# Optimization experiments

Measured on AMD Instinct MI355X. Metric: run time of the kernel, lower is better.

The kernel has to match this reference:

```python
import jax, jax.numpy as jnp
import numpy as np

VOCAB, EMB, HID = 5000, 16, 32
B, T = 256, 2048


def setup_inputs() -> dict:
    key = jax.random.key(0)
    k1, k2, k3, k4, k5 = jax.random.split(key, 5)
    tokens = jax.random.randint(k1, (B, T), 0, VOCAB, dtype=jnp.int32)
    emb = jax.random.normal(k2, (VOCAB, EMB), dtype=jnp.float32) * 0.05
    Wk = jax.random.normal(k3, (EMB, 4 * HID), dtype=jnp.float32) * 0.1
    Wr = jax.random.normal(k4, (HID, 4 * HID), dtype=jnp.float32) * 0.1
    b = jax.random.normal(k5, (4 * HID,), dtype=jnp.float32) * 0.1
    return {"tokens": tokens, "emb": emb, "Wk": Wk, "Wr": Wr, "b": b}


def reference(tokens, emb, Wk, Wr, b):
    # Embedding lookup: [B, T, EMB]
    x = emb[tokens]
    # Mask: Keras Masking on tiled token values -> masked where token == 0.
    mask = (tokens != 0)  # [B, T] True = valid step
    # Precompute input projections for all timesteps: [B, T, 4H]
    zx = jnp.einsum('bte,eh->bth', x, Wk) + b
    zx_t = jnp.swapaxes(zx, 0, 1)        # [T, B, 4H]
    mask_t = jnp.swapaxes(mask, 0, 1)    # [T, B]

    def step(carry, inp):
        h, c = carry
        z_x, m = inp
        z = z_x + h @ Wr                      # [B, 4H]
        i, f, g, o = jnp.split(z, 4, axis=-1) # Keras gate order i,f,g,o
        i = jax.nn.sigmoid(i)
        f = jax.nn.sigmoid(f)
        g = jnp.tanh(g)
        o = jax.nn.sigmoid(o)
        c_new = f * c + i * g
        h_new = o * jnp.tanh(c_new)
        m = m[:, None]
        # Keras masked RNN: masked steps carry forward previous state/output
        h = jnp.where(m, h_new, h)
        c = jnp.where(m, c_new, c)
        return (h, c), h

    h0 = jnp.zeros((tokens.shape[0], HID), dtype=zx.dtype)
    c0 = jnp.zeros((tokens.shape[0], HID), dtype=zx.dtype)
    _, hs = jax.lax.scan(step, (h0, c0), (zx_t, mask_t))
    return jnp.swapaxes(hs, 0, 1)  # [B, T, HID]
```

## Files before the change

### kernel.cpp

```cpp
#include <hip/hip_runtime.h>

#define G    128
#define HID  32
#define EMB  16
#define BB   256
#define TT   2048
#define VOC  5000

#define LOG2E      1.44269504088896340736f
#define TWOLOG2E   2.88539008177792681472f

typedef float v2f __attribute__((ext_vector_type(2)));
typedef __attribute__((ext_vector_type(8))) short short8;
typedef __attribute__((ext_vector_type(4))) float f32x4;

__device__ __forceinline__ float bf2f(unsigned short u) {
    return __uint_as_float(((unsigned)u) << 16);
}
__device__ __forceinline__ unsigned short f2bf(float f) {
    unsigned x = __float_as_uint(f);
    return (unsigned short)((x + 0x7FFFu + ((x >> 16) & 1u)) >> 16);
}
__device__ __forceinline__ float sigm2(float x) {
    const float e = __builtin_amdgcn_exp2f(-x);
    return __builtin_amdgcn_rcpf(1.f + e);
}
__device__ __forceinline__ float sigm(float x) {
    const float e = __expf(-x);
    return __builtin_amdgcn_rcpf(1.f + e);
}
__device__ __forceinline__ float tanh_f(float x) {
    const float e = __expf(-2.f * x);
    return (1.f - e) * __builtin_amdgcn_rcpf(1.f + e);
}
__device__ __forceinline__ float rdlf(float v, int k) {
    return __int_as_float(__builtin_amdgcn_readlane(__float_as_int(v), k));
}
template <int CTRL>
__device__ __forceinline__ unsigned dppq_u(unsigned v) {
    return (unsigned)__builtin_amdgcn_update_dpp(0, (int)v, CTRL, 0xF, 0xF, true);
}
template <int CTRL>
__device__ __forceinline__ float dppq_f(float v) {
    return __uint_as_float(dppq_u<CTRL>(__float_as_uint(v)));
}
#define DPP_XOR2   0x4E
#define DPP_BODD   0xF5
#define DPP_BEVN   0xA0
#define DPP_HMIRR  0x141
#define DPP_ROR8   0x128
#define DPP_MIRR   0x140

__device__ __host__ __forceinline__ int col_a(int l) {
    return (l >> 1) + 32 * (l & 1);
}

__global__ __launch_bounds__(64) void detect_kernel(
    const unsigned int* __restrict__ bias_w, int* __restrict__ flag)
{
    const int l = threadIdx.x;
    const unsigned u  = bias_w[l];
    const unsigned lo = u & 0xFFFFu;
    const float vlo = __uint_as_float(lo << 16);
    const float vhi = __uint_as_float(u & 0xFFFF0000u);
    const bool nz_even = (lo != 0u);
    const bool big = !(fabsf(vlo) < 1e6f) || !(fabsf(vhi) < 1e6f);
    const unsigned long long nz = __ballot(nz_even);
    const unsigned long long bg = __ballot(big);
    if (l == 0 && blockIdx.x == 0)
        *flag = (nz == 0ull || bg != 0ull) ? 1 : 0;
}

#define ZK_RPB 8
__global__ __launch_bounds__(64) void zk_kernel(
    const void* __restrict__ emb, const void* __restrict__ Wk,
    const void* __restrict__ bias, float* __restrict__ ZK,
    const int* __restrict__ flag)
{
    const int l  = threadIdx.x;
    const int v0 = blockIdx.x * ZK_RPB;
    const bool f32 = flag[0] != 0;
    const int ca = col_a(l), cb = ca + 64;
    const float sa = LOG2E;
    const float sb = ((l & 1) == 0) ? 2.f * LOG2E : LOG2E;

    float wa[EMB], wb[EMB], ba, bb;
    if (f32) {
        const float* W = (const float*)Wk;
        const float* B = (const float*)bias;
#pragma unroll
        for (int e = 0; e < EMB; ++e) { wa[e] = W[e * G + ca]; wb[e] = W[e * G + cb]; }
        ba = B[ca]; bb = B[cb];
    } else {
        const unsigned short* W = (const unsigned short*)Wk;
        const unsigned short* B = (const unsigned short*)bias;
#pragma unroll
        for (int e = 0; e < EMB; ++e) { wa[e] = bf2f(W[e * G + ca]); wb[e] = bf2f(W[e * G + cb]); }
        ba = bf2f(B[ca]); bb = bf2f(B[cb]);
    }

#pragma unroll
    for (int r = 0; r < ZK_RPB; ++r) {
        const int v = v0 + r;
        float x[EMB];
        if (f32) {
            const float* E = (const float*)emb + (size_t)v * EMB;
#pragma unroll
            for (int e = 0; e < EMB; ++e) x[e] = E[e];
        } else {
            const unsigned short* E = (const unsigned short*)emb + (size_t)v * EMB;
#pragma unroll
            for (int e = 0; e < EMB; ++e) x[e] = bf2f(E[e]);
        }
        float za = ba, zb = bb;
#pragma unroll
        for (int e = 0; e < EMB; ++e) {
            za = fmaf(x[e], wa[e], za);
            zb = fmaf(x[e], wb[e], zb);
        }
        ZK[(size_t)v * G + 2 * l]     = za * sa;
        ZK[(size_t)v * G + 2 * l + 1] = zb * sb;
    }
}

template <bool F32OUT>
__device__ __forceinline__ void scan_zk_loop(
    const int* __restrict__ trow, const float* __restrict__ ZK,
    void* __restrict__ orow, const short8 (&Bf)[8], int lane)
{
    const bool  h0  = (lane & 1) == 0;
    const float gm  = h0 ? 2.f : 1.f, ga = h0 ? -1.f : 0.f;
    const int   oj  = lane >> 1;
    const int   g4  = (lane >> 4) & 3;
    const bool  u_odd = (lane >> 1) & 1;
    const unsigned psel = u_odd ? 0x03020706u : 0x07060302u;
    const int   lm  = lane & 15;

    const f32x4 zc = {0.f, 0.f, 0.f, 0.f};
    float h = 0.f, c = 0.f;

    int tva = trow[lm];
    int tvb = trow[16 + lm];
    int tc[16], tn[16];
#pragma unroll
    for (int p = 0; p < 16; ++p) tc[p] = __builtin_amdgcn_readlane(tva, p);
#pragma unroll
    for (int p = 0; p < 16; ++p) tn[p] = __builtin_amdgcn_readlane(tvb, p);

    v2f pz[8];
#pragma unroll
    for (int d = 0; d < 8; ++d)
        pz[d] = *(const v2f*)(ZK + (size_t)tc[d] * G + 2 * lane);

    for (int cc = 0; cc < TT / 16; ++cc) {
        const int base = cc * 16;
        const int nxtc = (cc + 2 < TT / 16) ? (cc + 2) : (TT / 16 - 1);
        const int tvc = trow[nxtc * 16 + lm];
#pragma unroll
        for (int u = 0; u < 16; ++u) {
            const int t = base + u;
            const v2f z = pz[u & 7];
            {
                const int ptok = (u + 8 < 16) ? tc[u + 8] : tn[u - 8];
                pz[u & 7] = *(const v2f*)(ZK + (size_t)ptok * G + 2 * lane);
            }

            const unsigned rh  = __float_as_uint(h) + 0x8000u;
            const unsigned prt = dppq_u<DPP_XOR2>(rh);
            const unsigned pair = __builtin_amdgcn_perm(prt, rh, psel);
            const unsigned q1 = dppq_u<DPP_HMIRR>(pair);
            const unsigned q2 = dppq_u<DPP_ROR8 >(pair);
            const unsigned q3 = dppq_u<DPP_MIRR >(pair);
            union { unsigned u4[4]; short8 s8; } au;
            au.u4[0] = pair; au.u4[1] = q1; au.u4[2] = q2; au.u4[3] = q3;
            const short8 Af = au.s8;

            f32x4 d0 = __builtin_amdgcn_mfma_f32_16x16x32_bf16(Af, Bf[0], zc, 0, 0, 0);
            f32x4 d1 = __builtin_amdgcn_mfma_f32_16x16x32_bf16(Af, Bf[1], zc, 0, 0, 0);
            f32x4 d2 = __builtin_amdgcn_mfma_f32_16x16x32_bf16(Af, Bf[2], zc, 0, 0, 0);
            f32x4 d3 = __builtin_amdgcn_mfma_f32_16x16x32_bf16(Af, Bf[3], zc, 0, 0, 0);
            f32x4 d4 = __builtin_amdgcn_mfma_f32_16x16x32_bf16(Af, Bf[4], zc, 0, 0, 0);
            f32x4 d5 = __builtin_amdgcn_mfma_f32_16x16x32_bf16(Af, Bf[5], zc, 0, 0, 0);
            f32x4 d6 = __builtin_amdgcn_mfma_f32_16x16x32_bf16(Af, Bf[6], zc, 0, 0, 0);
            f32x4 d7 = __builtin_amdgcn_mfma_f32_16x16x32_bf16(Af, Bf[7], zc, 0, 0, 0);

            const float mva = (g4 < 2) ? (g4 == 0 ? d0.x : d1.x)
                                       : (g4 == 2 ? d2.x : d3.x);
            const float mvb = (g4 < 2) ? (g4 == 0 ? d4.x : d5.x)
                                       : (g4 == 2 ? d6.x : d7.x);
            const float za = z.x + mva;
            const float zb = z.y + mvb;

            const float aa1 = sigm2(za);
            const float s2  = sigm2(zb);
            const float aam = aa1 * gm;
            const float qc  = aa1 * ga;
            const float q   = fmaf(aam, s2, qc);
            const float fG  = dppq_f<DPP_BODD>(aa1);
            const float oG  = dppq_f<DPP_BODD>(s2);
            const float pr  = dppq_f<DPP_BEVN>(q);
            const float cN  = fmaf(fG, c, pr);

            const float ex = __builtin_amdgcn_exp2f(cN * TWOLOG2E);
            const float rr = __builtin_amdgcn_rcpf(ex + 1.f);
            const float oo = oG + oG;
            const float hN = fmaf(-oo, rr, oG);

            const bool m = tc[u] != 0;
            c = m ? cN : c;
            h = m ? hN : h;

            const int oi = t * HID + oj;
            if (F32OUT) __builtin_nontemporal_store(h, (float*)orow + oi);
            else        __builtin_nontemporal_store(f2bf(h), (unsigned short*)orow + oi);
        }
#pragma unroll
        for (int p = 0; p < 16; ++p) tc[p] = tn[p];
#pragma unroll
        for (int p = 0; p < 16; ++p) tn[p] = __builtin_amdgcn_readlane(tvc, p);
    }
}

__global__ __launch_bounds__(64) void scan_zk_kernel(
    const int* __restrict__ tokens, const float* __restrict__ ZK,
    const void* __restrict__ Wr, const void* __restrict__ bias,
    void* __restrict__ out, const int* __restrict__ flag)
{
    const int lane = threadIdx.x, b = blockIdx.x;
    const bool f32 = flag[0] != 0;

    short8 Bf[8];
    const int n  = lane & 15;
    const int k0 = (lane >> 4) * 8;
#pragma unroll
    for (int p = 0; p < 8; ++p) {
        const int ell = 16 * (p & 3) + n;
        const int col = (p < 4) ? col_a(ell) : (col_a(ell) + 64);
        const int jx  = (p & 3) << 1;
        const float sc = (p >= 4 && (n & 1) == 0) ? 2.f * LOG2E : LOG2E;
        short el[8];
        if (f32) {
            const float* W = (const float*)Wr;
#pragma unroll
            for (int j = 0; j < 8; ++j)
                el[j] = (short)f2bf(W[(k0 + (j ^ jx)) * G + col] * sc);
        } else {
            const unsigned short* W = (const unsigned short*)Wr;
#pragma unroll
            for (int j = 0; j < 8; ++j)
                el[j] = (short)f2bf(bf2f(W[(k0 + (j ^ jx)) * G + col]) * sc);
        }
        short8 s;
#pragma unroll
        for (int j = 0; j < 8; ++j) s[j] = el[j];
        Bf[p] = s;
    }

    const int* trow = tokens + (size_t)b * TT;
    if (f32) scan_zk_loop<true >(trow, ZK, (char*)out + (size_t)b * TT * HID * 4, Bf, lane);
    else     scan_zk_loop<false>(trow, ZK, (char*)out + (size_t)b * TT * HID * 2, Bf, lane);
}

template <bool F32>
__device__ __forceinline__ void row_load(const void* emb, int tok, uint4* r) {
    if (F32) { const uint4* p = (const uint4*)((const float*)emb + (size_t)tok*EMB);
               r[0]=p[0]; r[1]=p[1]; r[2]=p[2]; r[3]=p[3]; }
    else     { const uint4* p = (const uint4*)((const unsigned short*)emb + (size_t)tok*EMB);
               r[0]=p[0]; r[1]=p[1]; }
}
template <bool F32>
__device__ __forceinline__ void row_unpack(const uint4* r, float* x) {
    if (F32) {
        const unsigned w[16] = {r[0].x,r[0].y,r[0].z,r[0].w, r[1].x,r[1].y,r[1].z,r[1].w,
                                r[2].x,r[2].y,r[2].z,r[2].w, r[3].x,r[3].y,r[3].z,r[3].w};
#pragma unroll
        for (int e = 0; e < 16; ++e) x[e] = __uint_as_float(w[e]);
    } else {
        const unsigned w[8] = {r[0].x,r[0].y,r[0].z,r[0].w, r[1].x,r[1].y,r[1].z,r[1].w};
#pragma unroll
        for (int q = 0; q < 8; ++q) {
            x[2*q]   = __uint_as_float(w[q] << 16);
            x[2*q+1] = __uint_as_float(w[q] & 0xFFFF0000u);
        }
    }
}

template <bool F32>
__device__ __forceinline__ void scan_fused_loop(
    const int* __restrict__ trow, const void* __restrict__ emb, void* orow,
    const float (&wka)[EMB], const float (&wkb)[EMB],
    const float (&wra)[HID], const float (&wrb)[HID],
    float za0, float zb0, const int* tl, int lane)
{
    const bool  lo  = lane < HID;
    const float zsc = lo ? 2.f : 1.f, gm = lo ? 2.f : 1.f, ga = lo ? -1.f : 0.f;
    float h = 0.f, c = 0.f;
    uint4 praw[2][4];
    row_load<F32>(emb, trow[0], praw[0]);
    row_load<F32>(emb, trow[1], praw[1]);

    for (int tt = 0; tt < TT; tt += 2) {
#pragma unroll
        for (int u = 0; u < 2; ++u) {
            const int t = tt + u;
            float x[EMB];
            row_unpack<F32>(praw[u], x);
            int tn = t + 2; tn = tn > TT - 1 ? TT - 1 : tn;
            row_load<F32>(emb, tl[tn], praw[u]);
            float za = za0, zb = zb0;
#pragma unroll
            for (int e = 0; e < EMB; ++e) { za = fmaf(x[e], wka[e], za); zb = fmaf(x[e], wkb[e], zb); }
#pragma unroll
            for (int k = 0; k < HID; ++k) {
                const float hk = rdlf(h, k);
                za = fmaf(hk, wra[k], za);
                zb = fmaf(hk, wrb[k], zb);
            }
            const float a1 = sigm(za);
            const float s2 = sigm(zb * zsc);
            const float a2 = fmaf(s2, gm, ga);
            const float x1 = __shfl_xor(a1, 32);
            const float x2 = __shfl_xor(a2, 32);
            const float iV = lo ? a1 : x1, fV = lo ? x1 : a1;
            const float gV = lo ? a2 : x2, oV = lo ? x2 : a2;
            const float cN = fmaf(fV, c, iV * gV);
            const float hN = oV * tanh_f(cN);
            const bool  m  = tl[t] != 0;
            c = m ? cN : c;
            h = m ? hN : h;
            const int oi = t * HID + (lane & (HID - 1));
            if (F32) ((float*)orow)[oi] = h;
            else     ((unsigned short*)orow)[oi] = f2bf(h);
        }
    }
}

__global__ __launch_bounds__(64) void scan_fused_kernel(
    const int* __restrict__ tokens, const void* __restrict__ emb,
    const void* __restrict__ Wk, const void* __restrict__ Wr,
    const void* __restrict__ bias, void* __restrict__ out,
    const int* __restrict__ flag, int defmode)
{
    __shared__ int tl[TT];
    const int lane = threadIdx.x, b = blockIdx.x;
    const bool f32 = flag ? (flag[0] != 0) : (defmode != 0);
    const int* trow = tokens + (size_t)b * TT;
    for (int t = lane; t < TT; t += 64) tl[t] = trow[t];

    float wka[EMB], wkb[EMB], wra[HID], wrb[HID], za0, zb0;
    if (f32) {
        const float* WK = (const float*)Wk; const float* WR = (const float*)Wr;
        const float* B  = (const float*)bias;
#pragma unroll
        for (int e = 0; e < EMB; ++e) { wka[e] = WK[e*G + lane]; wkb[e] = WK[e*G + lane + 64]; }
#pragma unroll
        for (int k = 0; k < HID; ++k) { wra[k] = WR[k*G + lane]; wrb[k] = WR[k*G + lane + 64]; }
        za0 = B[lane]; zb0 = B[lane + 64];
    } else {
        const unsigned short* WK = (const unsigned short*)Wk;
        const unsigned short* WR = (const unsigned short*)Wr;
        const unsigned short* B  = (const unsigned short*)bias;
#pragma unroll
        for (int e = 0; e < EMB; ++e) { wka[e] = bf2f(WK[e*G + lane]); wkb[e] = bf2f(WK[e*G + lane + 64]); }
#pragma unroll
        for (int k = 0; k < HID; ++k) { wra[k] = bf2f(WR[k*G + lane]); wrb[k] = bf2f(WR[k*G + lane + 64]); }
        za0 = bf2f(B[lane]); zb0 = bf2f(B[lane + 64]);
    }
    __syncthreads();

    if (f32) scan_fused_loop<true >(trow, emb, (char*)out + (size_t)b*TT*HID*4,
                                    wka, wkb, wra, wrb, za0, zb0, tl, lane);
    else     scan_fused_loop<false>(trow, emb, (char*)out + (size_t)b*TT*HID*2,
                                    wka, wkb, wra, wrb, za0, zb0, tl, lane);
}

extern "C" void kernel_launch(void* const* d_in, const int* in_sizes, int n_in,
                              void* d_out, int out_size, void* d_ws, size_t ws_size,
                              hipStream_t stream) {
    const int*  tokens = (const int*)d_in[0];
    const void* emb    = d_in[1];
    const void* Wk     = d_in[2];
    const void* Wr     = d_in[3];
    const void* bias   = d_in[4];

    const size_t zk_off   = 256;
    const size_t zk_bytes = (size_t)VOC * G * sizeof(float);

    if (ws_size >= zk_off + zk_bytes) {
        int*   flag = (int*)d_ws;
        float* ZK   = (float*)((char*)d_ws + zk_off);
        detect_kernel<<<1, 64, 0, stream>>>((const unsigned int*)bias, flag);
        zk_kernel<<<VOC / ZK_RPB, 64, 0, stream>>>(emb, Wk, bias, ZK, flag);
        scan_zk_kernel<<<BB, 64, 0, stream>>>(tokens, ZK, Wr, bias, d_out, flag);
    } else if (ws_size >= 16) {
        int* flag = (int*)d_ws;
        detect_kernel<<<1, 64, 0, stream>>>((const unsigned int*)bias, flag);
        scan_fused_kernel<<<BB, 64, 0, stream>>>(tokens, emb, Wk, Wr, bias, d_out, flag, 1);
    } else {
        scan_fused_kernel<<<BB, 64, 0, stream>>>(tokens, emb, Wk, Wr, bias, d_out, nullptr, 1);
    }
}
```

Measured before the change: 441.4 us.

## Fold gate input into MFMA accumulator and simplify LSTM activation algebra

Passes the precomputed input projection as the MFMA accumulator instead of adding it afterward. The sigmoid/tanh algebra is reworked so the cell state is carried in a pre-scaled domain, folding the constants into ZK precompute and rcp offsets, which removes several multiplies and adds from the serial recurrence. The separate detect kernel is also removed: each kernel now checks the bias dtype inline with a wave ballot, dropping one launch and the flag round-trip. The rescaled cell state and bf16 MFMA rounding could shift numerics slightly.

Result: slower. 492.6 us (+11.6%).

```diff
diff --git a/kernel.cpp b/kernel.cpp
--- a/kernel.cpp
+++ b/kernel.cpp
@@ -21,10 +21,6 @@
     unsigned x = __float_as_uint(f);
     return (unsigned short)((x + 0x7FFFu + ((x >> 16) & 1u)) >> 16);
 }
-__device__ __forceinline__ float sigm2(float x) {
-    const float e = __builtin_amdgcn_exp2f(-x);
-    return __builtin_amdgcn_rcpf(1.f + e);
-}
 __device__ __forceinline__ float sigm(float x) {
     const float e = __expf(-x);
     return __builtin_amdgcn_rcpf(1.f + e);
@@ -55,11 +51,9 @@
     return (l >> 1) + 32 * (l & 1);
 }
 
-__global__ __launch_bounds__(64) void detect_kernel(
-    const unsigned int* __restrict__ bias_w, int* __restrict__ flag)
-{
-    const int l = threadIdx.x;
-    const unsigned u  = bias_w[l];
+__device__ __forceinline__ bool detect_f32(const unsigned* __restrict__ bias_w,
+                                           int lane) {
+    const unsigned u  = bias_w[lane];
     const unsigned lo = u & 0xFFFFu;
     const float vlo = __uint_as_float(lo << 16);
     const float vhi = __uint_as_float(u & 0xFFFF0000u);
@@ -67,21 +61,19 @@
     const bool big = !(fabsf(vlo) < 1e6f) || !(fabsf(vhi) < 1e6f);
     const unsigned long long nz = __ballot(nz_even);
     const unsigned long long bg = __ballot(big);
-    if (l == 0 && blockIdx.x == 0)
-        *flag = (nz == 0ull || bg != 0ull) ? 1 : 0;
+    return (nz == 0ull || bg != 0ull);
 }
 
 #define ZK_RPB 8
 __global__ __launch_bounds__(64) void zk_kernel(
     const void* __restrict__ emb, const void* __restrict__ Wk,
-    const void* __restrict__ bias, float* __restrict__ ZK,
-    const int* __restrict__ flag)
+    const void* __restrict__ bias, float* __restrict__ ZK)
 {
     const int l  = threadIdx.x;
     const int v0 = blockIdx.x * ZK_RPB;
-    const bool f32 = flag[0] != 0;
+    const bool f32 = detect_f32((const unsigned*)bias, l);
     const int ca = col_a(l), cb = ca + 64;
-    const float sa = LOG2E;
+    const float ba_add = ((l & 1) == 0) ? 1.f : 0.f;
     const float sb = ((l & 1) == 0) ? 2.f * LOG2E : LOG2E;
 
     float wa[EMB], wb[EMB], ba, bb;
@@ -118,8 +110,10 @@
             za = fmaf(x[e], wa[e], za);
             zb = fmaf(x[e], wb[e], zb);
         }
-        ZK[(size_t)v * G + 2 * l]     = za * sa;
-        ZK[(size_t)v * G + 2 * l + 1] = zb * sb;
+        v2f o2;
+        o2.x = fmaf(za, LOG2E, ba_add);
+        o2.y = zb * sb;
+        *(v2f*)(ZK + (size_t)v * G + 2 * l) = o2;
     }
 }
 
@@ -129,15 +123,14 @@
     void* __restrict__ orow, const short8 (&Bf)[8], int lane)
 {
     const bool  h0  = (lane & 1) == 0;
-    const float gm  = h0 ? 2.f : 1.f, ga = h0 ? -1.f : 0.f;
+    const float Kc  = h0 ? 0.5f : 1.0f;
     const int   oj  = lane >> 1;
     const int   g4  = (lane >> 4) & 3;
     const bool  u_odd = (lane >> 1) & 1;
     const unsigned psel = u_odd ? 0x03020706u : 0x07060302u;
     const int   lm  = lane & 15;
 
-    const f32x4 zc = {0.f, 0.f, 0.f, 0.f};
-    float h = 0.f, c = 0.f;
+    float h = 0.f, cS = 0.f;
 
     int tva = trow[lm];
     int tvb = trow[16 + lm];
@@ -175,40 +168,40 @@
             au.u4[0] = pair; au.u4[1] = q1; au.u4[2] = q2; au.u4[3] = q3;
             const short8 Af = au.s8;
 
-            f32x4 d0 = __builtin_amdgcn_mfma_f32_16x16x32_bf16(Af, Bf[0], zc, 0, 0, 0);
-            f32x4 d1 = __builtin_amdgcn_mfma_f32_16x16x32_bf16(Af, Bf[1], zc, 0, 0, 0);
-            f32x4 d2 = __builtin_amdgcn_mfma_f32_16x16x32_bf16(Af, Bf[2], zc, 0, 0, 0);
-            f32x4 d3 = __builtin_amdgcn_mfma_f32_16x16x32_bf16(Af, Bf[3], zc, 0, 0, 0);
-            f32x4 d4 = __builtin_amdgcn_mfma_f32_16x16x32_bf16(Af, Bf[4], zc, 0, 0, 0);
-            f32x4 d5 = __builtin_amdgcn_mfma_f32_16x16x32_bf16(Af, Bf[5], zc, 0, 0, 0);
-            f32x4 d6 = __builtin_amdgcn_mfma_f32_16x16x32_bf16(Af, Bf[6], zc, 0, 0, 0);
-            f32x4 d7 = __builtin_amdgcn_mfma_f32_16x16x32_bf16(Af, Bf[7], zc, 0, 0, 0);
-
+            const f32x4 Ca = {z.x, z.x, z.x, z.x};
+            const f32x4 Cb = {z.y, z.y, z.y, z.y};
+            f32x4 d0 = __builtin_amdgcn_mfma_f32_16x16x32_bf16(Af, Bf[0], Ca, 0, 0, 0);
+            f32x4 d1 = __builtin_amdgcn_mfma_f32_16x16x32_bf16(Af, Bf[1], Ca, 0, 0, 0);
+            f32x4 d2 = __builtin_amdgcn_mfma_f32_16x16x32_bf16(Af, Bf[2], Ca, 0, 0, 0);
+            f32x4 d3 = __builtin_amdgcn_mfma_f32_16x16x32_bf16(Af, Bf[3], Ca, 0, 0, 0);
+            f32x4 d4 = __builtin_amdgcn_mfma_f32_16x16x32_bf16(Af, Bf[4], Cb, 0, 0, 0);
+            f32x4 d5 = __builtin_amdgcn_mfma_f32_16x16x32_bf16(Af, Bf[5], Cb, 0, 0, 0);
+            f32x4 d6 = __builtin_amdgcn_mfma_f32_16x16x32_bf16(Af, Bf[6], Cb, 0, 0, 0);
+            f32x4 d7 = __builtin_amdgcn_mfma_f32_16x16x32_bf16(Af, Bf[7], Cb, 0, 0, 0);
+
+            const float mvb = (g4 < 2) ? (g4 == 0 ? d4.x : d5.x)
+                                       : (g4 == 2 ? d6.x : d7.x);
             const float mva = (g4 < 2) ? (g4 == 0 ? d0.x : d1.x)
                                        : (g4 == 2 ? d2.x : d3.x);
-            const float mvb = (g4 < 2) ? (g4 == 0 ? d4.x : d5.x)
-                                       : (g4 == 2 ? d6.x : d7.x);
-            const float za = z.x + mva;
-            const float zb = z.y + mvb;
-
-            const float aa1 = sigm2(za);
-            const float s2  = sigm2(zb);
-            const float aam = aa1 * gm;
-            const float qc  = aa1 * ga;
-            const float q   = fmaf(aam, s2, qc);
-            const float fG  = dppq_f<DPP_BODD>(aa1);
+
+            const float exa = __builtin_amdgcn_exp2f(-mva);
+            const float exb = __builtin_amdgcn_exp2f(-mvb);
+            const float r1  = __builtin_amdgcn_rcpf(exa + Kc);
+            const float s2  = __builtin_amdgcn_rcpf(exb + 1.f);
+            const float s2p = fmaf(s2, -TWOLOG2E, LOG2E);
+            const float q   = r1 * s2p;
+            const float fc  = dppq_f<DPP_BODD>(r1) * cS;
+            const float cN  = dppq_f<DPP_BEVN>(q) + fc;
             const float oG  = dppq_f<DPP_BODD>(s2);
-            const float pr  = dppq_f<DPP_BEVN>(q);
-            const float cN  = fmaf(fG, c, pr);
-
-            const float ex = __builtin_amdgcn_exp2f(cN * TWOLOG2E);
-            const float rr = __builtin_amdgcn_rcpf(ex + 1.f);
-            const float oo = oG + oG;
-            const float hN = fmaf(-oo, rr, oG);
+
+            const float exh = __builtin_amdgcn_exp2f(cN);
+            const float rr  = __builtin_amdgcn_rcpf(exh + 1.f);
+            const float oo  = oG + oG;
+            const float hN  = fmaf(oo, rr, -oG);
 
             const bool m = tc[u] != 0;
-            c = m ? cN : c;
-            h = m ? hN : h;
+            cS = m ? cN : cS;
+            h  = m ? hN : h;
 
             const int oi = t * HID + oj;
             if (F32OUT) __builtin_nontemporal_store(h, (float*)orow + oi);
@@ -224,10 +217,10 @@
 __global__ __launch_bounds__(64) void scan_zk_kernel(
     const int* __restrict__ tokens, const float* __restrict__ ZK,
     const void* __restrict__ Wr, const void* __restrict__ bias,
-    void* __restrict__ out, const int* __restrict__ flag)
+    void* __restrict__ out)
 {
     const int lane = threadIdx.x, b = blockIdx.x;
-    const bool f32 = flag[0] != 0;
+    const bool f32 = detect_f32((const unsigned*)bias, lane);
 
     short8 Bf[8];
     const int n  = lane & 15;
@@ -338,12 +331,11 @@
 __global__ __launch_bounds__(64) void scan_fused_kernel(
     const int* __restrict__ tokens, const void* __restrict__ emb,
     const void* __restrict__ Wk, const void* __restrict__ Wr,
-    const void* __restrict__ bias, void* __restrict__ out,
-    const int* __restrict__ flag, int defmode)
+    const void* __restrict__ bias, void* __restrict__ out)
 {
     __shared__ int tl[TT];
     const int lane = threadIdx.x, b = blockIdx.x;
-    const bool f32 = flag ? (flag[0] != 0) : (defmode != 0);
+    const bool f32 = detect_f32((const unsigned*)bias, lane);
     const int* trow = tokens + (size_t)b * TT;
     for (int t = lane; t < TT; t += 64) tl[t] = trow[t];
 
@@ -387,16 +379,10 @@
     const size_t zk_bytes = (size_t)VOC * G * sizeof(float);
 
     if (ws_size >= zk_off + zk_bytes) {
-        int*   flag = (int*)d_ws;
-        float* ZK   = (float*)((char*)d_ws + zk_off);
-        detect_kernel<<<1, 64, 0, stream>>>((const unsigned int*)bias, flag);
-        zk_kernel<<<VOC / ZK_RPB, 64, 0, stream>>>(emb, Wk, bias, ZK, flag);
-        scan_zk_kernel<<<BB, 64, 0, stream>>>(tokens, ZK, Wr, bias, d_out, flag);
-    } else if (ws_size >= 16) {
-        int* flag = (int*)d_ws;
-        detect_kernel<<<1, 64, 0, stream>>>((const unsigned int*)bias, flag);
-        scan_fused_kernel<<<BB, 64, 0, stream>>>(tokens, emb, Wk, Wr, bias, d_out, flag, 1);
+        float* ZK = (float*)((char*)d_ws + zk_off);
+        zk_kernel<<<VOC / ZK_RPB, 64, 0, stream>>>(emb, Wk, bias, ZK);
+        scan_zk_kernel<<<BB, 64, 0, stream>>>(tokens, ZK, Wr, bias, d_out);
     } else {
-        scan_fused_kernel<<<BB, 64, 0, stream>>>(tokens, emb, Wk, Wr, bias, d_out, nullptr, 1);
-    }
-}
+        scan_fused_kernel<<<BB, 64, 0, stream>>>(tokens, emb, Wk, Wr, bias, d_out);
+    }
+}
```
